# Kernel tuning notes

Measured on AMD Instinct MI355X. Metric: run time of the kernel, lower is better.

## Reference

```python
import jax, jax.numpy as jnp
import numpy as np

EMBED = 1024
B, T = 4, 2048

def setup_inputs() -> dict:
    key = jax.random.key(0)
    k1, k2, k3, k4, k5 = jax.random.split(key, 5)
    s_in = 1.0 / np.sqrt(EMBED)
    return {
        "x": jax.random.normal(k1, (B, T, EMBED), dtype=jnp.float32),
        "w_qkv": jax.random.normal(k2, (3 * EMBED, EMBED), dtype=jnp.float32) * s_in,  # torch Linear layout [out,in]
        "b_qkv": jax.random.normal(k3, (3 * EMBED,), dtype=jnp.float32) * 0.01,
        "w_proj": jax.random.normal(k4, (EMBED, EMBED), dtype=jnp.float32) * s_in,
        "b_proj": jax.random.normal(k5, (EMBED,), dtype=jnp.float32) * 0.01,
    }

def reference(x, w_qkv, b_qkv, w_proj, b_proj):
    Bq, Tq, C = x.shape
    qkv = jnp.einsum('btc,oc->bto', x, w_qkv) + b_qkv        # [B,T,3C]
    q, k, v = jnp.split(qkv, 3, axis=-1)                      # each [B,T,C]
    att = jnp.einsum('btc,bsc->bts', q, k) / jnp.sqrt(jnp.float32(C))  # [B,T,T]
    causal = jnp.tril(jnp.ones((Tq, Tq), dtype=bool))
    att = jnp.where(causal[None, :, :], att, -jnp.inf)
    att = jax.nn.softmax(att, axis=-1)
    out = jnp.einsum('bts,bsc->btc', att, v)                   # [B,T,C]
    return jnp.einsum('btc,oc->bto', out, w_proj) + b_proj
```

## Files before the change

kernel.cpp:

```cpp
#include <hip/hip_runtime.h>
#include <hip/hip_bf16.h>

typedef __hip_bfloat16 bf16;
typedef __attribute__((ext_vector_type(8))) short bf16x8;
typedef __attribute__((ext_vector_type(4))) float f32x4;

#define GLD16(gp, lp) __builtin_amdgcn_global_load_lds( \
    (const __attribute__((address_space(1))) void*)(gp), \
    (__attribute__((address_space(3))) void*)(lp), 16, 0, 0)

__global__ __launch_bounds__(256) void cvt_bf16(const float* __restrict__ in,
                                                bf16* __restrict__ out) {
    int i = (blockIdx.x * 256 + threadIdx.x) * 4;
    float4 f = *(const float4*)&in[i];
    __hip_bfloat162 p0, p1;
    p0.x = __float2bfloat16(f.x); p0.y = __float2bfloat16(f.y);
    p1.x = __float2bfloat16(f.z); p1.y = __float2bfloat16(f.w);
    *(__hip_bfloat162*)&out[i]     = p0;
    *(__hip_bfloat162*)&out[i + 2] = p1;
}

__global__ void transpose_v(const bf16* __restrict__ V, bf16* __restrict__ Vt) {
    __shared__ bf16 tile[32][33];
    const int b = blockIdx.z;
    const int c0 = blockIdx.x * 32, t0 = blockIdx.y * 32;
    const int tx = threadIdx.x, ty = threadIdx.y;
    #pragma unroll
    for (int i = 0; i < 32; i += 8)
        tile[ty + i][tx] = V[((size_t)(b * 2048 + t0 + ty + i)) * 1024 + c0 + tx];
    __syncthreads();
    #pragma unroll
    for (int i = 0; i < 32; i += 8)
        Vt[((size_t)b * 1024 + c0 + ty + i) * 2048 + t0 + tx] = tile[tx][ty + i];
}

__global__ __launch_bounds__(256) void softmax_causal(float* __restrict__ S) {
    const int row = blockIdx.x;
    const int t = row & 2047;
    float* srow = S + (size_t)row * 2048;
    bf16* prow = (bf16*)srow;
    const int tid = threadIdx.x;
    const int base = tid * 8;
    float4 f0 = *(const float4*)&srow[base];
    float4 f1 = *(const float4*)&srow[base + 4];
    float v[8] = {f0.x, f0.y, f0.z, f0.w, f1.x, f1.y, f1.z, f1.w};
    float lmax = -INFINITY;
    #pragma unroll
    for (int i = 0; i < 8; ++i) {
        v[i] = (base + i <= t) ? v[i] : -INFINITY;
        lmax = fmaxf(lmax, v[i]);
    }
    #pragma unroll
    for (int off = 32; off; off >>= 1) lmax = fmaxf(lmax, __shfl_xor(lmax, off));
    __shared__ float red[4];
    const int wave = tid >> 6, lane = tid & 63;
    if (lane == 0) red[wave] = lmax;
    __syncthreads();
    lmax = fmaxf(fmaxf(red[0], red[1]), fmaxf(red[2], red[3]));
    float lsum = 0.f;
    #pragma unroll
    for (int i = 0; i < 8; ++i) { v[i] = __expf(v[i] - lmax); lsum += v[i]; }
    #pragma unroll
    for (int off = 32; off; off >>= 1) lsum += __shfl_xor(lsum, off);
    __syncthreads();
    if (lane == 0) red[wave] = lsum;
    __syncthreads();
    lsum = red[0] + red[1] + red[2] + red[3];
    const float inv = 1.f / lsum;
    #pragma unroll
    for (int i = 0; i < 8; ++i) prow[base + i] = __float2bfloat16(v[i] * inv);
}

__global__ __launch_bounds__(256) void gemm_bt(
    int mode,
    const bf16* __restrict__ A, int lda, size_t batchA,
    const bf16* __restrict__ B, int ldb, size_t batchB,
    int K,
    const float* __restrict__ bias,
    void* __restrict__ out0, void* __restrict__ out1, void* __restrict__ out2)
{
    constexpr int BK = 32;
    __shared__ bf16 As[128][BK];
    __shared__ bf16 Bs[128][BK];

    const int bx = blockIdx.x, by = blockIdx.y, bz = blockIdx.z;
    if (mode == 1 && bx > by) return;
    const int m0 = by * 128, n0 = bx * 128;
    const int keff = (mode == 2) ? (by + 1) * 128 : K;

    const bf16* Ab = A + (size_t)bz * batchA;
    const bf16* Bb = B + (size_t)bz * batchB;

    const int tid = threadIdx.x;
    const int lane = tid & 63;
    const int wave = tid >> 6;
    const int wm = (wave >> 1) * 64;
    const int wn = (wave & 1) * 64;

    f32x4 acc[4][4] = {};

    for (int k0 = 0; k0 < keff; k0 += BK) {
        #pragma unroll
        for (int p = 0; p < 2; ++p) {
            int idx = p * 256 + tid;
            int r = idx >> 2;
            int kc = (idx & 3) * 8;
            GLD16(Ab + (size_t)(m0 + r) * lda + (k0 + kc), &As[r][kc]);
            GLD16(Bb + (size_t)(n0 + r) * ldb + (k0 + kc), &Bs[r][kc]);
        }
        __syncthreads();

        bf16x8 af[4], bfr[4];
        #pragma unroll
        for (int m = 0; m < 4; ++m)
            af[m] = *(const bf16x8*)&As[wm + m * 16 + (lane & 15)][(lane >> 4) * 8];
        #pragma unroll
        for (int n = 0; n < 4; ++n)
            bfr[n] = *(const bf16x8*)&Bs[wn + n * 16 + (lane & 15)][(lane >> 4) * 8];
        #pragma unroll
        for (int m = 0; m < 4; ++m)
            #pragma unroll
            for (int n = 0; n < 4; ++n)
                acc[m][n] = __builtin_amdgcn_mfma_f32_16x16x32_bf16(
                    af[m], bfr[n], acc[m][n], 0, 0, 0);
        __syncthreads();
    }

    #pragma unroll
    for (int m = 0; m < 4; ++m) {
        #pragma unroll
        for (int n = 0; n < 4; ++n) {
            #pragma unroll
            for (int j = 0; j < 4; ++j) {
                const int gr = m0 + wm + m * 16 + ((lane >> 4) << 2) + j;
                const int gc = n0 + wn + n * 16 + (lane & 15);
                float v = acc[m][n][j];
                if (mode == 0) {
                    v += bias[gc];
                    const int which = gc >> 10;
                    const int col = gc & 1023;
                    bf16* dst = which == 0 ? (bf16*)out0
                              : which == 1 ? (bf16*)out1 : (bf16*)out2;
                    dst[(size_t)gr * 1024 + col] = __float2bfloat16(v);
                } else if (mode == 1) {
                    ((float*)out0)[(size_t)bz * (2048ull * 2048) +
                                   (size_t)gr * 2048 + gc] = v * 0.03125f;
                } else if (mode == 2) {
                    ((bf16*)out0)[((size_t)bz * 2048 + gr) * 1024 + gc] =
                        __float2bfloat16(v);
                } else {
                    ((float*)out0)[(size_t)gr * 1024 + gc] = v + bias[gc];
                }
            }
        }
    }
}

extern "C" void kernel_launch(void* const* d_in, const int* in_sizes, int n_in,
                              void* d_out, int out_size, void* d_ws, size_t ws_size,
                              hipStream_t stream) {
    const float* x      = (const float*)d_in[0];
    const float* w_qkv  = (const float*)d_in[1];
    const float* b_qkv  = (const float*)d_in[2];
    const float* w_proj = (const float*)d_in[3];
    const float* b_proj = (const float*)d_in[4];
    float* out = (float*)d_out;
    char* ws = (char*)d_ws;

    bf16* Xb = (bf16*)(ws);
    bf16* Wq = (bf16*)(ws + 16777216);
    bf16* Wp = (bf16*)(ws + 23068672);
    bf16* Qb = (bf16*)(ws + 25165824);
    bf16* Kb = (bf16*)(ws + 41943040);
    bf16* Vb = (bf16*)(ws + 58720256);
    float* S = (float*)(ws + 75497472);
    bf16* Vt = Xb;
    bf16* O  = Qb;

    hipLaunchKernelGGL(cvt_bf16, dim3(8192), dim3(256), 0, stream, x, Xb);
    hipLaunchKernelGGL(cvt_bf16, dim3(3072), dim3(256), 0, stream, w_qkv, Wq);
    hipLaunchKernelGGL(cvt_bf16, dim3(1024), dim3(256), 0, stream, w_proj, Wp);

    hipLaunchKernelGGL(gemm_bt, dim3(24, 64, 1), dim3(256), 0, stream,
        0, Xb, 1024, (size_t)0, Wq, 1024, (size_t)0, 1024, b_qkv,
        (void*)Qb, (void*)Kb, (void*)Vb);

    hipLaunchKernelGGL(transpose_v, dim3(32, 64, 4), dim3(32, 8), 0, stream, Vb, Vt);

    hipLaunchKernelGGL(gemm_bt, dim3(16, 16, 4), dim3(256), 0, stream,
        1, Qb, 1024, (size_t)(2048ull * 1024), Kb, 1024, (size_t)(2048ull * 1024),
        1024, (const float*)nullptr, (void*)S, (void*)nullptr, (void*)nullptr);

    hipLaunchKernelGGL(softmax_causal, dim3(8192), dim3(256), 0, stream, S);

    hipLaunchKernelGGL(gemm_bt, dim3(8, 16, 4), dim3(256), 0, stream,
        2, (const bf16*)S, 4096, (size_t)(2048ull * 4096), Vt, 2048,
        (size_t)(1024ull * 2048), 2048, (const float*)nullptr,
        (void*)O, (void*)nullptr, (void*)nullptr);

    hipLaunchKernelGGL(gemm_bt, dim3(8, 64, 1), dim3(256), 0, stream,
        3, O, 1024, (size_t)0, Wp, 1024, (size_t)0, 1024, b_proj,
        (void*)out, (void*)nullptr, (void*)nullptr);
}
```

Baseline: 376.0 us.

## Add double-buffered 256x256 swizzled GEMM for QKV, QK^T and output projection

```diff
diff --git a/kernel.cpp b/kernel.cpp
--- a/kernel.cpp
+++ b/kernel.cpp
@@ -156,6 +156,130 @@
     }
 }
 
+template<int MODE>
+__global__ __launch_bounds__(512, 2) void gemm256(
+    const bf16* __restrict__ A, const bf16* __restrict__ B,
+    const float* __restrict__ bias,
+    void* __restrict__ out0, void* __restrict__ out1, void* __restrict__ out2)
+{
+    __shared__ bf16 As[2][256][64];
+    __shared__ bf16 Bs[2][256][64];
+    constexpr int NT = 16;
+
+    const int bx = blockIdx.x, by = blockIdx.y, bz = blockIdx.z;
+    if (MODE == 1 && bx > by) return;
+    const int m0 = by * 256, n0 = bx * 256;
+
+    const bf16* Ab = A + (MODE == 1 ? (size_t)bz * (2048ull * 1024) : 0);
+    const bf16* Bb = B + (MODE == 1 ? (size_t)bz * (2048ull * 1024) : 0);
+
+    const int tid = threadIdx.x;
+    const int lane = tid & 63, wave = tid >> 6;
+    const int wr = wave >> 2, wc = wave & 3;
+    const int frow = lane & 15, fk = lane >> 4, fx = lane & 7;
+
+    const int rl = tid >> 3;
+    const int scol = ((tid & 7) ^ (rl & 7)) * 8;
+    const bf16* pAsrc = Ab + (size_t)(m0 + rl) * 1024 + scol;
+    const bf16* pBsrc = Bb + (size_t)(n0 + rl) * 1024 + scol;
+    const int dchunk = tid * 8;
+
+    f32x4 acc[4][4][2] = {};
+
+    #define STG(P, LDSBASE, H, K0) do { \
+        GLD16((P) + (size_t)(H) * 128 * 1024 + (K0), (LDSBASE) + (H) * 8192 + dchunk); \
+        GLD16((P) + (size_t)((H) * 128 + 64) * 1024 + (K0), (LDSBASE) + (H) * 8192 + 4096 + dchunk); \
+    } while (0)
+
+    {
+        bf16* la = &As[0][0][0]; bf16* lb = &Bs[0][0][0];
+        STG(pAsrc, la, 0, 0);
+        STG(pBsrc, lb, 0, 0);
+        STG(pBsrc, lb, 1, 0);
+        STG(pAsrc, la, 1, 0);
+    }
+
+    for (int t = 0; t < NT; ++t) {
+        const int buf = t & 1, nbuf = buf ^ 1;
+        const int kn = (t + 1) * 64;
+        bf16* lan = &As[nbuf][0][0]; bf16* lbn = &Bs[nbuf][0][0];
+        const bool more = (t + 1 < NT);
+
+        #pragma unroll
+        for (int q = 0; q < 4; ++q) {
+            if (more) {
+                if (q == 0)      STG(pAsrc, lan, 0, kn);
+                else if (q == 1) STG(pBsrc, lbn, 0, kn);
+                else if (q == 2) STG(pBsrc, lbn, 1, kn);
+                else             STG(pAsrc, lan, 1, kn);
+                if (q < 3) asm volatile("s_waitcnt vmcnt(6)" ::: "memory");
+            } else {
+                if (q == 0)      asm volatile("s_waitcnt vmcnt(4)" ::: "memory");
+                else if (q == 1) asm volatile("s_waitcnt vmcnt(2)" ::: "memory");
+                else if (q == 2) asm volatile("s_waitcnt vmcnt(0)" ::: "memory");
+            }
+            __builtin_amdgcn_s_barrier();
+
+            const int aR = ((q >> 1) << 7) + wr * 64 + frow;
+            const int bR = ((q & 1) << 7) + wc * 32 + frow;
+            bf16x8 av[4][2], bv[2][2];
+            #pragma unroll
+            for (int m = 0; m < 4; ++m)
+                #pragma unroll
+                for (int ks = 0; ks < 2; ++ks)
+                    av[m][ks] = *(const bf16x8*)
+                        &As[buf][aR + m * 16][((((ks << 2) | fk) ^ fx) << 3)];
+            #pragma unroll
+            for (int n = 0; n < 2; ++n)
+                #pragma unroll
+                for (int ks = 0; ks < 2; ++ks)
+                    bv[n][ks] = *(const bf16x8*)
+                        &Bs[buf][bR + n * 16][((((ks << 2) | fk) ^ fx) << 3)];
+
+            __builtin_amdgcn_s_setprio(1);
+            #pragma unroll
+            for (int m = 0; m < 4; ++m)
+                #pragma unroll
+                for (int n = 0; n < 2; ++n)
+                    #pragma unroll
+                    for (int ks = 0; ks < 2; ++ks)
+                        acc[q][m][n] = __builtin_amdgcn_mfma_f32_16x16x32_bf16(
+                            av[m][ks], bv[n][ks], acc[q][m][n], 0, 0, 0);
+            __builtin_amdgcn_s_setprio(0);
+        }
+    }
+    #undef STG
+
+    #pragma unroll
+    for (int q = 0; q < 4; ++q) {
+        #pragma unroll
+        for (int m = 0; m < 4; ++m) {
+            #pragma unroll
+            for (int n = 0; n < 2; ++n) {
+                #pragma unroll
+                for (int j = 0; j < 4; ++j) {
+                    const int gr = m0 + ((q >> 1) << 7) + wr * 64 + m * 16 + (fk << 2) + j;
+                    const int gc = n0 + ((q & 1) << 7) + wc * 32 + n * 16 + frow;
+                    float v = acc[q][m][n][j];
+                    if (MODE == 0) {
+                        v += bias[gc];
+                        const int which = gc >> 10;
+                        const int col = gc & 1023;
+                        bf16* dst = which == 0 ? (bf16*)out0
+                                  : which == 1 ? (bf16*)out1 : (bf16*)out2;
+                        dst[(size_t)gr * 1024 + col] = __float2bfloat16(v);
+                    } else if (MODE == 1) {
+                        ((float*)out0)[(size_t)bz * (2048ull * 2048) +
+                                       (size_t)gr * 2048 + gc] = v * 0.03125f;
+                    } else {
+                        ((float*)out0)[(size_t)gr * 1024 + gc] = v + bias[gc];
+                    }
+                }
+            }
+        }
+    }
+}
+
 extern "C" void kernel_launch(void* const* d_in, const int* in_sizes, int n_in,
                               void* d_out, int out_size, void* d_ws, size_t ws_size,
                               hipStream_t stream) {
@@ -181,15 +305,13 @@
     hipLaunchKernelGGL(cvt_bf16, dim3(3072), dim3(256), 0, stream, w_qkv, Wq);
     hipLaunchKernelGGL(cvt_bf16, dim3(1024), dim3(256), 0, stream, w_proj, Wp);
 
-    hipLaunchKernelGGL(gemm_bt, dim3(24, 64, 1), dim3(256), 0, stream,
-        0, Xb, 1024, (size_t)0, Wq, 1024, (size_t)0, 1024, b_qkv,
-        (void*)Qb, (void*)Kb, (void*)Vb);
+    gemm256<0><<<dim3(12, 32, 1), 512, 0, stream>>>(
+        Xb, Wq, b_qkv, (void*)Qb, (void*)Kb, (void*)Vb);
 
     hipLaunchKernelGGL(transpose_v, dim3(32, 64, 4), dim3(32, 8), 0, stream, Vb, Vt);
 
-    hipLaunchKernelGGL(gemm_bt, dim3(16, 16, 4), dim3(256), 0, stream,
-        1, Qb, 1024, (size_t)(2048ull * 1024), Kb, 1024, (size_t)(2048ull * 1024),
-        1024, (const float*)nullptr, (void*)S, (void*)nullptr, (void*)nullptr);
+    gemm256<1><<<dim3(8, 8, 4), 512, 0, stream>>>(
+        Qb, Kb, (const float*)nullptr, (void*)S, nullptr, nullptr);
 
     hipLaunchKernelGGL(softmax_causal, dim3(8192), dim3(256), 0, stream, S);
 
@@ -198,7 +320,6 @@
         (size_t)(1024ull * 2048), 2048, (const float*)nullptr,
         (void*)O, (void*)nullptr, (void*)nullptr);
 
-    hipLaunchKernelGGL(gemm_bt, dim3(8, 64, 1), dim3(256), 0, stream,
-        3, O, 1024, (size_t)0, Wp, 1024, (size_t)0, 1024, b_proj,
-        (void*)out, (void*)nullptr, (void*)nullptr);
-}
+    gemm256<3><<<dim3(4, 32, 1), 512, 0, stream>>>(
+        O, Wp, b_proj, (void*)out, nullptr, nullptr);
+}
```

New measurement: 339.1 us. 9.8% less time.
